# Optimization experiments

Measured on AMD Instinct MI355X. Metric: run time of the kernel, lower is better.

## Reference

```python
import jax, jax.numpy as jnp
import numpy as np
import math

CS = 8       # cell_size
NBINS = 8
SIGMA = 1.0
IMG = 224
BATCH = 256
TWO_PI = 2.0 * math.pi


def setup_inputs() -> dict:
    key = jax.random.key(0)
    x = jax.random.normal(key, (BATCH, 3, IMG, IMG), dtype=jnp.float32)
    coords = jnp.arange(CS, dtype=jnp.float32) - (CS - 1) / 2.0
    xx, yy = jnp.meshgrid(coords, coords, indexing='ij')
    gauss = jnp.exp(-(xx ** 2 + yy ** 2) / (2.0 * SIGMA ** 2)).reshape(1, CS * CS)
    kx = jnp.array([[-1., 0., 1.], [-2., 0., 2.], [-1., 0., 1.]], dtype=jnp.float32).reshape(1, 1, 3, 3)
    ky = jnp.array([[-1., -2., -1.], [0., 0., 0.], [1., 2., 1.]], dtype=jnp.float32).reshape(1, 1, 3, 3)
    return {"x": x, "gauss": gauss, "kx": kx, "ky": ky}


def _conv(im, k):
    # NCHW conv, padding=1, stride=1 (matches F.conv2d(..., padding=1))
    return jax.lax.conv_general_dilated(
        im, k, window_strides=(1, 1), padding=[(1, 1), (1, 1)],
        dimension_numbers=('NCHW', 'OIHW', 'NCHW'))


def reference(x, gauss, kx, ky):
    bs, _, H, W = x.shape
    gray = 0.2989 * x[:, 0:1] + 0.587 * x[:, 1:2] + 0.114 * x[:, 2:3]  # [bs,1,H,W]
    gx = _conv(gray, kx)
    gy = _conv(gray, ky)
    mag = jnp.sqrt(gx ** 2 + gy ** 2 + 1e-6)
    ang = jnp.mod(jnp.arctan2(gy, gx), TWO_PI)
    Hc, Wc = H // CS, W // CS
    n_cells = Hc * Wc

    def to_cells(a):
        # [bs,1,H,W] -> [bs*n_cells, CS*CS], within-cell order (kh,kw) row-major
        # matching F.unfold's kernel-position ordering.
        return a.reshape(bs, Hc, CS, Wc, CS).transpose(0, 1, 3, 2, 4).reshape(bs * n_cells, CS * CS)

    mags = to_cells(mag) * gauss  # gauss broadcasts over kernel positions
    angs = to_cells(ang)

    bin_w = TWO_PI / NBINS
    idx = (angs / bin_w).astype(jnp.int32) % NBINS  # [bs*n_cells, CS*CS]

    N = bs * n_cells
    hist = jnp.zeros((N, NBINS), dtype=mags.dtype)
    hist = hist.at[jnp.arange(N)[:, None], idx].add(mags)  # scatter_add per cell
    hist = hist.reshape(bs, n_cells * NBINS)
    hist = hist / (jnp.linalg.norm(hist, axis=1, keepdims=True) + 1e-6)
    return hist
```

## Files before the change

### kernel.cpp

```cpp
#include <hip/hip_runtime.h>
#include <math.h>

#define CS 8
#define NBINS 8
#define IMG 224
#define HC 28
#define CELLS (HC*HC)
#define OUTPER (CELLS*NBINS)
#define BATCH 256

__global__ void hog_zero_kernel(float* __restrict__ sumsq) {
    int t = threadIdx.x;
    if (t < BATCH) sumsq[t] = 0.f;
}

__global__ __launch_bounds__(256) void hog_hist_kernel(
    const float* __restrict__ x, const float* __restrict__ gauss,
    float* __restrict__ out, float* __restrict__ sumsq)
{
    const int b   = blockIdx.x;
    const int cr  = blockIdx.y;
    const int tid = threadIdx.x;

    __shared__ float g[10][226];
    __shared__ float hist[HC * NBINS];
    __shared__ float gw[64];
    __shared__ float wsum[4];

    if (tid < HC * NBINS) hist[tid] = 0.f;
    if (tid < 64) gw[tid] = gauss[tid];
    if (tid < 20) {
        int rr = tid >> 1, cc = (tid & 1) ? 225 : 0;
        g[rr][cc] = 0.f;
    }

    const int r0 = cr * CS;
    const size_t plane = (size_t)IMG * IMG;
    const float* xb = x + (size_t)b * 3 * plane;

    if (tid < IMG) {
        const int c = tid;
        #pragma unroll
        for (int rr = 0; rr < 10; ++rr) {
            int gr = r0 - 1 + rr;
            float val = 0.f;
            if (gr >= 0 && gr < IMG) {
                size_t off = (size_t)gr * IMG + c;
                float rch = xb[off];
                float gch = xb[plane + off];
                float bch = xb[2 * plane + off];
                val = 0.2989f * rch + 0.587f * gch + 0.114f * bch;
            }
            g[rr][c + 1] = val;
        }
    }
    __syncthreads();

    if (tid < IMG) {
        const int c  = tid;
        const int cc = c >> 3;
        const int wc = c & 7;
        #pragma unroll
        for (int ir = 0; ir < CS; ++ir) {
            const int lr = ir + 1;
            float a00 = g[lr-1][c], a01 = g[lr-1][c+1], a02 = g[lr-1][c+2];
            float a10 = g[lr  ][c],                     a12 = g[lr  ][c+2];
            float a20 = g[lr+1][c], a21 = g[lr+1][c+1], a22 = g[lr+1][c+2];
            float gx = (a02 - a00) + 2.f * (a12 - a10) + (a22 - a20);
            float gy = (a20 - a00) + 2.f * (a21 - a01) + (a22 - a02);
            float mag = sqrtf(gx * gx + gy * gy + 1e-6f);

            float ax = fabsf(gx), ay = fabsf(gy);
            int bin;
            if (gy > 0.f) {
                if (gx > 0.f)        bin = (gy < gx) ? 0 : 1;
                else if (gx == 0.f)  bin = 2;
                else                 bin = (ay > ax) ? 2 : 3;
            } else if (gy == 0.f) {
                bin = (gx < 0.f) ? 4 : 0;
            } else {
                if (gx < 0.f)        bin = (ay < ax) ? 4 : 5;
                else if (gx == 0.f)  bin = 6;
                else                 bin = (ay > ax) ? 6 : 7;
            }
            float w = gw[ir * 8 + wc];
            atomicAdd(&hist[cc * NBINS + bin], w * mag);
        }
    }
    __syncthreads();

    float s = 0.f;
    if (tid < HC * NBINS) {
        float h = hist[tid];
        out[(size_t)b * OUTPER + (size_t)cr * (HC * NBINS) + tid] = h;
        s = h * h;
    }
    #pragma unroll
    for (int o = 32; o > 0; o >>= 1) s += __shfl_down(s, o, 64);
    if ((tid & 63) == 0) wsum[tid >> 6] = s;
    __syncthreads();
    if (tid == 0) {
        float t = wsum[0] + wsum[1] + wsum[2] + wsum[3];
        atomicAdd(&sumsq[b], t);
    }
}

__global__ __launch_bounds__(256) void hog_norm_kernel(
    float* __restrict__ out, const float* __restrict__ sumsq)
{
    int i = blockIdx.x * blockDim.x + threadIdx.x;
    const int vec_per_img = OUTPER / 4;
    if (i >= BATCH * vec_per_img) return;
    int b = i / vec_per_img;
    float n = sqrtf(sumsq[b]) + 1e-6f;
    float4* o4 = (float4*)out;
    float4 v = o4[i];
    v.x = v.x / n;
    v.y = v.y / n;
    v.z = v.z / n;
    v.w = v.w / n;
    o4[i] = v;
}

extern "C" void kernel_launch(void* const* d_in, const int* in_sizes, int n_in,
                              void* d_out, int out_size, void* d_ws, size_t ws_size,
                              hipStream_t stream) {
    const float* x     = (const float*)d_in[0];
    const float* gauss = (const float*)d_in[1];
    float* out   = (float*)d_out;
    float* sumsq = (float*)d_ws;

    hog_zero_kernel<<<1, 256, 0, stream>>>(sumsq);
    dim3 grid(BATCH, HC);
    hog_hist_kernel<<<grid, 256, 0, stream>>>(x, gauss, out, sumsq);
    hog_norm_kernel<<<(BATCH * OUTPER / 4 + 255) / 256, 256, 0, stream>>>(out, sumsq);
}
```

Before: 278.2 us.

## Process two cell rows per block with register histograms and vectorized loads

Each block now covers 16 image rows (two cell rows), which lowers the halo reload overhead from 10/8 to 18/16 rows. Grayscale input is loaded with float4 reads into a padded shared tile. The shared-memory atomic histogram is replaced by per-thread register bins that are reduced with xor shuffles across the 8 lanes of each cell, and the results are written directly to the output. A 3x3 sliding register window reuses rows between iterations. The costs are more registers per thread and half as many blocks.

Result: faster. 244.4 us (-12.2%).

```diff
diff --git a/kernel.cpp b/kernel.cpp
--- a/kernel.cpp
+++ b/kernel.cpp
@@ -5,13 +5,15 @@
 #define NBINS 8
 #define IMG 224
 #define HC 28
-#define CELLS (HC*HC)
-#define OUTPER (CELLS*NBINS)
+#define OUTPER (HC*HC*NBINS)
 #define BATCH 256
+#define RS 16
+#define GR (RS + 2)
+#define GSTRIDE 232
+#define GOFF 4
 
 __global__ void hog_zero_kernel(float* __restrict__ sumsq) {
-    int t = threadIdx.x;
-    if (t < BATCH) sumsq[t] = 0.f;
+    if (threadIdx.x < BATCH) sumsq[threadIdx.x] = 0.f;
 }
 
 __global__ __launch_bounds__(256) void hog_hist_kernel(
@@ -19,90 +21,103 @@
     float* __restrict__ out, float* __restrict__ sumsq)
 {
     const int b   = blockIdx.x;
-    const int cr  = blockIdx.y;
+    const int by  = blockIdx.y;
     const int tid = threadIdx.x;
+    const int r0  = by * RS;
 
-    __shared__ float g[10][226];
-    __shared__ float hist[HC * NBINS];
-    __shared__ float gw[64];
+    __shared__ float g[GR][GSTRIDE];
     __shared__ float wsum[4];
 
-    if (tid < HC * NBINS) hist[tid] = 0.f;
-    if (tid < 64) gw[tid] = gauss[tid];
-    if (tid < 20) {
-        int rr = tid >> 1, cc = (tid & 1) ? 225 : 0;
+    const size_t plane = (size_t)IMG * IMG;
+    const float* xb = x + (size_t)b * 3 * plane;
+
+    if (tid < GR * 2) {
+        int rr = tid >> 1, cc = (tid & 1) ? (GOFF + IMG) : (GOFF - 1);
         g[rr][cc] = 0.f;
     }
 
-    const int r0 = cr * CS;
-    const size_t plane = (size_t)IMG * IMG;
-    const float* xb = x + (size_t)b * 3 * plane;
-
-    if (tid < IMG) {
-        const int c = tid;
-        #pragma unroll
-        for (int rr = 0; rr < 10; ++rr) {
-            int gr = r0 - 1 + rr;
-            float val = 0.f;
-            if (gr >= 0 && gr < IMG) {
-                size_t off = (size_t)gr * IMG + c;
-                float rch = xb[off];
-                float gch = xb[plane + off];
-                float bch = xb[2 * plane + off];
-                val = 0.2989f * rch + 0.587f * gch + 0.114f * bch;
-            }
-            g[rr][c + 1] = val;
+    for (int idx = tid; idx < GR * (IMG / 4); idx += 256) {
+        int row = idx / (IMG / 4), c4 = idx % (IMG / 4);
+        int gr = r0 - 1 + row;
+        float4 val = make_float4(0.f, 0.f, 0.f, 0.f);
+        if (gr >= 0 && gr < IMG) {
+            const float* base = xb + (size_t)gr * IMG;
+            float4 R = ((const float4*)base)[c4];
+            float4 G = ((const float4*)(base + plane))[c4];
+            float4 B = ((const float4*)(base + 2 * plane))[c4];
+            val.x = 0.2989f * R.x + 0.587f * G.x + 0.114f * B.x;
+            val.y = 0.2989f * R.y + 0.587f * G.y + 0.114f * B.y;
+            val.z = 0.2989f * R.z + 0.587f * G.z + 0.114f * B.z;
+            val.w = 0.2989f * R.w + 0.587f * G.w + 0.114f * B.w;
         }
+        *(float4*)&g[row][GOFF + c4 * 4] = val;
     }
     __syncthreads();
 
+    float ssq = 0.f;
     if (tid < IMG) {
         const int c  = tid;
-        const int cc = c >> 3;
         const int wc = c & 7;
+
+        float wgt[8];
         #pragma unroll
-        for (int ir = 0; ir < CS; ++ir) {
-            const int lr = ir + 1;
-            float a00 = g[lr-1][c], a01 = g[lr-1][c+1], a02 = g[lr-1][c+2];
-            float a10 = g[lr  ][c],                     a12 = g[lr  ][c+2];
-            float a20 = g[lr+1][c], a21 = g[lr+1][c+1], a22 = g[lr+1][c+2];
-            float gx = (a02 - a00) + 2.f * (a12 - a10) + (a22 - a20);
-            float gy = (a20 - a00) + 2.f * (a21 - a01) + (a22 - a02);
+        for (int i = 0; i < 8; ++i) wgt[i] = gauss[i * 8 + wc];
+
+        float h[8];
+        #pragma unroll
+        for (int k = 0; k < 8; ++k) h[k] = 0.f;
+
+        auto dump = [&](int crow) {
+            #pragma unroll
+            for (int s = 1; s < 8; s <<= 1) {
+                #pragma unroll
+                for (int k = 0; k < 8; ++k) h[k] += __shfl_xor(h[k], s, 64);
+            }
+            float v = (wc < 4) ? ((wc < 2) ? (wc == 0 ? h[0] : h[1])
+                                          : (wc == 2 ? h[2] : h[3]))
+                               : ((wc < 6) ? (wc == 4 ? h[4] : h[5])
+                                          : (wc == 6 ? h[6] : h[7]));
+            out[(size_t)b * OUTPER + (size_t)crow * (HC * NBINS) + c] = v;
+            ssq += v * v;
+            #pragma unroll
+            for (int k = 0; k < 8; ++k) h[k] = 0.f;
+        };
+
+        float t0 = g[0][c + 3], t1 = g[0][c + 4], t2 = g[0][c + 5];
+        float m0 = g[1][c + 3], m1 = g[1][c + 4], m2 = g[1][c + 5];
+
+        #pragma unroll
+        for (int sr = 0; sr < RS; ++sr) {
+            float b0 = g[sr + 2][c + 3], b1 = g[sr + 2][c + 4], b2 = g[sr + 2][c + 5];
+            float gx = (t2 - t0) + 2.f * (m2 - m0) + (b2 - b0);
+            float gy = (b0 - t0) + 2.f * (b1 - t1) + (b2 - t2);
             float mag = sqrtf(gx * gx + gy * gy + 1e-6f);
+            float ax = fabsf(gx), ay = fabsf(gy);
 
-            float ax = fabsf(gx), ay = fabsf(gy);
             int bin;
-            if (gy > 0.f) {
-                if (gx > 0.f)        bin = (gy < gx) ? 0 : 1;
-                else if (gx == 0.f)  bin = 2;
-                else                 bin = (ay > ax) ? 2 : 3;
-            } else if (gy == 0.f) {
-                bin = (gx < 0.f) ? 4 : 0;
-            } else {
-                if (gx < 0.f)        bin = (ay < ax) ? 4 : 5;
-                else if (gx == 0.f)  bin = 6;
-                else                 bin = (ay > ax) ? 6 : 7;
-            }
-            float w = gw[ir * 8 + wc];
-            atomicAdd(&hist[cc * NBINS + bin], w * mag);
+            if (gy > 0.f)       bin = (gx > 0.f)  ? ((gy < gx) ? 0 : 1)
+                                    : (gx == 0.f) ? 2 : ((ay > ax) ? 2 : 3);
+            else if (gy == 0.f) bin = (gx < 0.f) ? 4 : 0;
+            else                bin = (gx < 0.f)  ? ((ay < ax) ? 4 : 5)
+                                    : (gx == 0.f) ? 6 : ((ay > ax) ? 6 : 7);
+
+            float wm = wgt[sr & 7] * mag;
+            #pragma unroll
+            for (int k = 0; k < 8; ++k) h[k] += (bin == k) ? wm : 0.f;
+
+            t0 = m0; t1 = m1; t2 = m2;
+            m0 = b0; m1 = b1; m2 = b2;
+
+            if (sr == 7)       dump(2 * by);
+            else if (sr == 15) dump(2 * by + 1);
         }
     }
+
+    #pragma unroll
+    for (int o = 32; o > 0; o >>= 1) ssq += __shfl_down(ssq, o, 64);
+    if ((tid & 63) == 0) wsum[tid >> 6] = ssq;
     __syncthreads();
-
-    float s = 0.f;
-    if (tid < HC * NBINS) {
-        float h = hist[tid];
-        out[(size_t)b * OUTPER + (size_t)cr * (HC * NBINS) + tid] = h;
-        s = h * h;
-    }
-    #pragma unroll
-    for (int o = 32; o > 0; o >>= 1) s += __shfl_down(s, o, 64);
-    if ((tid & 63) == 0) wsum[tid >> 6] = s;
-    __syncthreads();
-    if (tid == 0) {
-        float t = wsum[0] + wsum[1] + wsum[2] + wsum[3];
-        atomicAdd(&sumsq[b], t);
-    }
+    if (tid == 0) atomicAdd(&sumsq[b], wsum[0] + wsum[1] + wsum[2] + wsum[3]);
 }
 
 __global__ __launch_bounds__(256) void hog_norm_kernel(
@@ -115,10 +130,7 @@
     float n = sqrtf(sumsq[b]) + 1e-6f;
     float4* o4 = (float4*)out;
     float4 v = o4[i];
-    v.x = v.x / n;
-    v.y = v.y / n;
-    v.z = v.z / n;
-    v.w = v.w / n;
+    v.x /= n; v.y /= n; v.z /= n; v.w /= n;
     o4[i] = v;
 }
 
@@ -131,7 +143,7 @@
     float* sumsq = (float*)d_ws;
 
     hog_zero_kernel<<<1, 256, 0, stream>>>(sumsq);
-    dim3 grid(BATCH, HC);
+    dim3 grid(BATCH, IMG / RS);
     hog_hist_kernel<<<grid, 256, 0, stream>>>(x, gauss, out, sumsq);
     hog_norm_kernel<<<(BATCH * OUTPER / 4 + 255) / 256, 256, 0, stream>>>(out, sumsq);
 }
```
